# Kernel optimization log

Measured on AMD Instinct MI355X. Metric: run time of the kernel, lower is better.

## Reference

```python
import jax, jax.numpy as jnp
import numpy as np

NUM_GROUPS = 8
EPS = 1e-5


def setup_inputs() -> dict:
    key = jax.random.key(0)
    ks = jax.random.split(key, 3)
    B, C, H, W = 32, 256, 64, 64
    x = jax.random.normal(ks[0], (B, C, H, W), dtype=jnp.float32)
    gn_weight = jnp.ones((C,), dtype=jnp.float32)
    gn_bias = jnp.zeros((C,), dtype=jnp.float32)
    # 1x1 convs stored as [out_ch, in_ch] matrices (kernel dims squeezed)
    qkv_weight = jax.random.normal(ks[1], (3 * C, C), dtype=jnp.float32) * (1.0 / np.sqrt(C))
    qkv_bias = jnp.zeros((3 * C,), dtype=jnp.float32)
    proj_weight = jax.random.normal(ks[2], (C, C), dtype=jnp.float32) * (1.0 / np.sqrt(C))
    proj_bias = jnp.zeros((C,), dtype=jnp.float32)
    return {
        "x": x,
        "gn_weight": gn_weight,
        "gn_bias": gn_bias,
        "qkv_weight": qkv_weight,
        "qkv_bias": qkv_bias,
        "proj_weight": proj_weight,
        "proj_bias": proj_bias,
    }


def _group_norm(x, weight, bias):
    B, C, H, W = x.shape
    g = x.reshape(B, NUM_GROUPS, C // NUM_GROUPS, H, W)
    mean = g.mean(axis=(2, 3, 4), keepdims=True)
    var = g.var(axis=(2, 3, 4), keepdims=True)
    g = (g - mean) * jax.lax.rsqrt(var + EPS)
    x = g.reshape(B, C, H, W)
    return x * weight[None, :, None, None] + bias[None, :, None, None]


def reference(x, gn_weight, gn_bias, qkv_weight, qkv_bias, proj_weight, proj_bias):
    B, C, H, W = x.shape
    x_norm = _group_norm(x, gn_weight, gn_bias)
    # 1x1 conv C -> 3C: contraction over channel dim
    qkv = jnp.einsum('bchw,oc->bohw', x_norm, qkv_weight) + qkv_bias[None, :, None, None]
    qkv = qkv.reshape(B, 3, C, H * W)  # [B,3,C,HW]
    q, k, v = qkv[:, 0], qkv[:, 1], qkv[:, 2]  # each [B,C,HW]
    # channel attention: attn is [B,C,C], softmax over last (key-channel) dim
    scale = 1.0 / jnp.sqrt(jnp.asarray(C, dtype=x.dtype))
    scores = jnp.einsum('bcn,bdn->bcd', q, k) * scale
    attn = jax.nn.softmax(scores, axis=-1)
    out = jnp.einsum('bcd,bdn->bcn', attn, v).reshape(B, C, H, W)
    proj = jnp.einsum('bchw,oc->bohw', out, proj_weight) + proj_bias[None, :, None, None]
    return x + proj
```

## Files before the change

kernel.cpp:

```cpp
#include <hip/hip_runtime.h>


#define B_ 32
#define C_ 256
#define N_ 4096
#define GSIZE (32 * N_)
#define EPSV 1e-5f
#define SCALE 0.0625f

#define OFF_SC    0
#define OFF_SH    8192
#define OFF_RS    16384
#define OFF_RSP   24576
#define OFF_SQP   90112
#define OFF_RALL  155648
#define OFF_CV    180224
#define OFF_CONST 188416
#define OFF_WVT   196608
#define OFF_GM    229376
#define OFF_AT    2326528
#define OFF_S16   4423680
#define OFF_GP    5472256

typedef _Float16 half_t;
typedef half_t f16x8 __attribute__((ext_vector_type(8)));
typedef float f32x16 __attribute__((ext_vector_type(16)));

__global__ __launch_bounds__(512, 1) void gram_v4_k(const float* __restrict__ x,
                                                    float* __restrict__ ws) {
  __shared__ __align__(16) char hb[2][32768];
  int b = blockIdx.x >> 3, ks = blockIdx.x & 7;
  int t = threadIdx.x;
  const float* xb = x + (size_t)b * (C_ * (size_t)N_) + ks * 512;
  int lane = t & 63, w = t >> 6;
  int wm = w >> 2, wn = w & 3, r31 = lane & 31, hi = lane >> 5;
  int lrow = t >> 4, lc4 = t & 15;
  const float* lbase = xb + (size_t)lrow * N_ + lc4 * 4;
  f32x16 acc[4][2] = {};
  float4 stg[2][8];
  float rs[8] = {0.f, 0.f, 0.f, 0.f, 0.f, 0.f, 0.f, 0.f};
  float rq[8] = {0.f, 0.f, 0.f, 0.f, 0.f, 0.f, 0.f, 0.f};

#define LOADV(sb, c)                                                      \
  _Pragma("unroll") for (int p = 0; p < 8; ++p)                           \
      stg[sb][p] = *(const float4*)(lbase + (size_t)p * 32 * N_ + (c) * 64);

#define WRITEV(sb, buf)                                                   \
  {                                                                       \
    char* bp = hb[buf];                                                   \
    _Pragma("unroll") for (int p = 0; p < 8; ++p) {                       \
      float4 v = stg[sb][p];                                              \
      rs[p] += v.x + v.y + v.z + v.w;                                     \
      rq[p] += v.x * v.x + v.y * v.y + v.z * v.z + v.w * v.w;             \
      union { half_t h[4]; uint2 u; } H;                                  \
      H.h[0] = (half_t)v.x; H.h[1] = (half_t)v.y;                         \
      H.h[2] = (half_t)v.z; H.h[3] = (half_t)v.w;                         \
      int row = lrow + p * 32;                                            \
      int slot = (lc4 >> 1) ^ (row & 7);                                  \
      *(uint2*)(bp + row * 128 + slot * 16 + (lc4 & 1) * 8) = H.u;        \
    }                                                                     \
  }

  LOADV(0, 0);
  LOADV(1, 1);
  WRITEV(0, 0);
  __syncthreads();
  for (int c = 0; c < 8; ++c) {
    int buf = c & 1;
#pragma unroll
    for (int kk = 0; kk < 4; ++kk) {
      int kb = kk * 32 + hi * 16;
      f16x8 Af[4], Bf[2];
#pragma unroll
      for (int m = 0; m < 4; ++m) {
        int row = wm * 128 + m * 32 + r31;
        Af[m] = *(const f16x8*)(hb[buf] + row * 128 + (((kb >> 4) ^ (row & 7)) * 16));
      }
#pragma unroll
      for (int n = 0; n < 2; ++n) {
        int row = wn * 64 + n * 32 + r31;
        Bf[n] = *(const f16x8*)(hb[buf] + row * 128 + (((kb >> 4) ^ (row & 7)) * 16));
      }
#pragma unroll
      for (int m = 0; m < 4; ++m)
#pragma unroll
        for (int n = 0; n < 2; ++n)
          acc[m][n] = __builtin_amdgcn_mfma_f32_32x32x16_f16(Af[m], Bf[n], acc[m][n], 0, 0, 0);
    }
    if (c < 7) {
      int nb = (c + 1) & 1;
      WRITEV(nb, nb);
      if (c < 6) LOADV(buf, c + 2);
      __syncthreads();
    }
  }
#pragma unroll
  for (int p = 0; p < 8; ++p) {
    float s = rs[p], q = rq[p];
    s += __shfl_xor(s, 1); s += __shfl_xor(s, 2);
    s += __shfl_xor(s, 4); s += __shfl_xor(s, 8);
    q += __shfl_xor(q, 1); q += __shfl_xor(q, 2);
    q += __shfl_xor(q, 4); q += __shfl_xor(q, 8);
    if ((t & 15) == 0) {
      int row = lrow + p * 32;
      ws[OFF_RSP + (size_t)blockIdx.x * 256 + row] = s;
      ws[OFF_SQP + (size_t)blockIdx.x * 256 + row] = q;
    }
  }
  half_t* Gp = (half_t*)(ws + OFF_GP) + (size_t)blockIdx.x * 65536;
#pragma unroll
  for (int m = 0; m < 4; ++m)
#pragma unroll
    for (int n = 0; n < 2; ++n)
#pragma unroll
      for (int r = 0; r < 16; ++r) {
        int gr = wm * 128 + m * 32 + (r & 3) + 8 * (r >> 2) + 4 * hi;
        int gc = wn * 64 + n * 32 + r31;
        Gp[gr * 256 + gc] = (half_t)acc[m][n][r];
      }
#undef LOADV
#undef WRITEV
}

__global__ __launch_bounds__(256) void gsum_k(float* __restrict__ ws) {
  int bx = blockIdx.x;
  int b = bx >> 6, seg = bx & 63;
  int e0 = seg * 1024 + threadIdx.x * 4;
  const half_t* Gp = (const half_t*)(ws + OFF_GP) + (size_t)b * 8 * 65536 + e0;
  float4 s = {0.f, 0.f, 0.f, 0.f};
#pragma unroll
  for (int ks = 0; ks < 8; ++ks) {
    union { uint2 u; half_t h[4]; } P;
    P.u = *(const uint2*)(Gp + (size_t)ks * 65536);
    s.x += (float)P.h[0]; s.y += (float)P.h[1];
    s.z += (float)P.h[2]; s.w += (float)P.h[3];
  }
  *(float4*)(ws + OFF_GM + (size_t)b * 65536 + e0) = s;
}

__global__ __launch_bounds__(256) void prep_k(const float* __restrict__ gw,
                                              const float* __restrict__ gb,
                                              const float* __restrict__ qkvw,
                                              float* __restrict__ ws) {
  int b = blockIdx.x, t = threadIdx.x;
  __shared__ float sL[256], qL[256], svecs[256], gmean[8], grstd[8];
  float s = 0.f, q = 0.f;
#pragma unroll
  for (int ks = 0; ks < 8; ++ks) {
    s += ws[OFF_RSP + (b * 8 + ks) * 256 + t];
    q += ws[OFF_SQP + (b * 8 + ks) * 256 + t];
  }
  ws[OFF_RS + b * 256 + t] = s;
  sL[t] = s; qL[t] = q;
  __syncthreads();
  if (t < 8) {
    float gs = 0.f, gq = 0.f;
    for (int i = 0; i < 32; ++i) { gs += sL[t * 32 + i]; gq += qL[t * 32 + i]; }
    float mean = gs * (1.f / GSIZE);
    float var = gq * (1.f / GSIZE) - mean * mean;
    gmean[t] = mean;
    grstd[t] = rsqrtf(var + EPSV);
  }
  __syncthreads();
  int g = t >> 5;
  float sc = grstd[g] * gw[t];
  float sh = gb[t] - gmean[g] * sc;
  ws[OFF_SC + b * 256 + t] = sc;
  ws[OFF_SH + b * 256 + t] = sh;
  float sv = s * sc + 4096.f * sh;
  svecs[t] = sv;
  __syncthreads();
  for (int oo = 0; oo < 3; ++oo) {
    int o = t + oo * 256;
    const float* wr = qkvw + (size_t)o * 256;
    float acc = 0.f;
#pragma unroll 8
    for (int c = 0; c < 256; ++c) acc += wr[c] * svecs[c];
    ws[OFF_RALL + b * 768 + o] = acc;
  }
}

__global__ __launch_bounds__(256) void wvt_k(const float* __restrict__ qkvw,
                                             float* __restrict__ ws) {
  int e = blockIdx.x, d = threadIdx.x;
  float v = qkvw[(size_t)(512 + d) * 256 + e];
  ((half_t*)(ws + OFF_WVT))[e * 256 + d] = (half_t)v;
}

__global__ __launch_bounds__(256) void fused_logits_k(
    const float* __restrict__ qkvw, const float* __restrict__ qkvb,
    float* __restrict__ ws) {
  int b = blockIdx.y, r0 = blockIdx.x * 32;
  int t = threadIdx.x, lane = t & 63, w = t >> 6, r31 = lane & 31, hi = lane >> 5;
  __shared__ __align__(16) char GHL[32768];
  __shared__ __align__(16) char AHL[8192];
  __shared__ float T1s[32][257];
  __shared__ float scs[256], shs[256], rss[256];
  __shared__ float bk_s[256], rk_s[256], bq_s[32], rq_s[32];
  scs[t] = ws[OFF_SC + b * 256 + t];
  shs[t] = ws[OFF_SH + b * 256 + t];
  rss[t] = ws[OFF_RS + b * 256 + t];
  bk_s[t] = qkvb[256 + t];
  rk_s[t] = ws[OFF_RALL + b * 768 + 256 + t];
  if (t < 32) {
    bq_s[t] = qkvb[r0 + t];
    rq_s[t] = ws[OFF_RALL + b * 768 + r0 + t];
  }
  __syncthreads();
  const float* Graw = ws + OFF_GM + (size_t)b * 65536;
  f32x16 acc[2] = {};
  for (int k0 = 0; k0 < 256; k0 += 32) {
    {
      int row = t >> 3, c4 = t & 7;
      float4 v = *(const float4*)(qkvw + (size_t)(r0 + row) * 256 + k0 + c4 * 4);
      union { half_t h[4]; uint2 u; } H, L;
      float vv[4] = {v.x, v.y, v.z, v.w};
#pragma unroll
      for (int j = 0; j < 4; ++j) {
        half_t h = (half_t)vv[j];
        H.h[j] = h; L.h[j] = (half_t)(vv[j] - (float)h);
      }
      int s8 = row & 7;
      *(uint2*)(AHL + row * 128 + (((c4 >> 1) ^ s8) * 16) + (c4 & 1) * 8) = H.u;
      *(uint2*)(AHL + row * 128 + ((((c4 >> 1) + 4) ^ s8) * 16) + (c4 & 1) * 8) = L.u;
    }
    {
#pragma unroll
      for (int p = 0; p < 8; ++p) {
        int f = t + p * 256;
        int row = f >> 3, c4 = f & 7;
        float4 gv = *(const float4*)(Graw + (size_t)row * 256 + k0 + c4 * 4);
        float scd = scs[row], shd = shs[row], rsd = rss[row];
        union { half_t h[4]; uint2 u; } H, L;
        float gvv[4] = {gv.x, gv.y, gv.z, gv.w};
#pragma unroll
        for (int j = 0; j < 4; ++j) {
          int cc = k0 + c4 * 4 + j;
          float scc = scs[cc], shc = shs[cc];
          float val = scc * scd * gvv[j] + scc * shd * rss[cc] +
                      shc * scd * rsd + 4096.f * shc * shd;
          half_t h = (half_t)val;
          H.h[j] = h; L.h[j] = (half_t)(val - (float)h);
        }
        int s8 = row & 7;
        *(uint2*)(GHL + row * 128 + (((c4 >> 1) ^ s8) * 16) + (c4 & 1) * 8) = H.u;
        *(uint2*)(GHL + row * 128 + ((((c4 >> 1) + 4) ^ s8) * 16) + (c4 & 1) * 8) = L.u;
      }
    }
    __syncthreads();
#pragma unroll
    for (int kk = 0; kk < 2; ++kk) {
      int kb = kk * 32 + hi * 16;
      int arow = r31;
      f16x8 Aq = *(const f16x8*)(AHL + arow * 128 + (((kb >> 4) ^ (arow & 7)) * 16));
#pragma unroll
      for (int n = 0; n < 2; ++n) {
        int row = w * 64 + n * 32 + r31;
        int s8 = row & 7;
        f16x8 Bh = *(const f16x8*)(GHL + row * 128 + (((kb >> 4) ^ s8) * 16));
        f16x8 Bl = *(const f16x8*)(GHL + row * 128 + ((((kb >> 4) + 4) ^ s8) * 16));
        acc[n] = __builtin_amdgcn_mfma_f32_32x32x16_f16(Aq, Bh, acc[n], 0, 0, 0);
        acc[n] = __builtin_amdgcn_mfma_f32_32x32x16_f16(Aq, Bl, acc[n], 0, 0, 0);
      }
    }
    __syncthreads();
  }
#pragma unroll
  for (int n = 0; n < 2; ++n)
#pragma unroll
    for (int r = 0; r < 16; ++r)
      T1s[(r & 3) + 8 * (r >> 2) + 4 * hi][w * 64 + n * 32 + r31] = acc[n][r];
  __syncthreads();
  f32x16 acc2[2] = {};
  for (int k0 = 0; k0 < 256; k0 += 64) {
    {
      int row = t >> 3;
#pragma unroll
      for (int u = 0; u < 2; ++u) {
        int c4 = (t & 7) + u * 8;
        float vv[4];
#pragma unroll
        for (int j = 0; j < 4; ++j) vv[j] = T1s[row][k0 + c4 * 4 + j];
        union { half_t h[4]; uint2 u2; } H, L;
#pragma unroll
        for (int j = 0; j < 4; ++j) {
          half_t h = (half_t)vv[j];
          H.h[j] = h; L.h[j] = (half_t)(vv[j] - (float)h);
        }
        int s16 = row & 15;
        *(uint2*)(AHL + row * 256 + (((c4 >> 1) ^ s16) * 16) + (c4 & 1) * 8) = H.u2;
        *(uint2*)(AHL + row * 256 + ((((c4 >> 1) + 8) ^ s16) * 16) + (c4 & 1) * 8) = L.u2;
      }
    }
    {
#pragma unroll
      for (int p = 0; p < 16; ++p) {
        int f = t + p * 256;
        int row = f >> 4, c4 = f & 15;
        float4 v = *(const float4*)(qkvw + (size_t)(256 + row) * 256 + k0 + c4 * 4);
        union { half_t h[4]; uint2 u; } H;
        H.h[0] = (half_t)v.x; H.h[1] = (half_t)v.y;
        H.h[2] = (half_t)v.z; H.h[3] = (half_t)v.w;
        int slot = (c4 >> 1) ^ (row & 7);
        *(uint2*)(GHL + row * 128 + slot * 16 + (c4 & 1) * 8) = H.u;
      }
    }
    __syncthreads();
#pragma unroll
    for (int kk = 0; kk < 4; ++kk) {
      int kb = kk * 32 + hi * 16;
      int arow = r31;
      int s16 = arow & 15;
      f16x8 Ah = *(const f16x8*)(AHL + arow * 256 + (((kb >> 4) ^ s16) * 16));
      f16x8 Al = *(const f16x8*)(AHL + arow * 256 + ((((kb >> 4) + 8) ^ s16) * 16));
#pragma unroll
      for (int n = 0; n < 2; ++n) {
        int row = w * 64 + n * 32 + r31;
        f16x8 Bf = *(const f16x8*)(GHL + row * 128 + (((kb >> 4) ^ (row & 7)) * 16));
        acc2[n] = __builtin_amdgcn_mfma_f32_32x32x16_f16(Ah, Bf, acc2[n], 0, 0, 0);
        acc2[n] = __builtin_amdgcn_mfma_f32_32x32x16_f16(Al, Bf, acc2[n], 0, 0, 0);
      }
    }
    __syncthreads();
  }
#pragma unroll
  for (int n = 0; n < 2; ++n)
#pragma unroll
    for (int r = 0; r < 16; ++r) {
      int rr = (r & 3) + 8 * (r >> 2) + 4 * hi;
      int cc = w * 64 + n * 32 + r31;
      float v = acc2[n][r];
      v = (v + bq_s[rr] * rk_s[cc] + bk_s[cc] * rq_s[rr] +
           4096.f * bq_s[rr] * bk_s[cc]) * SCALE;
      T1s[rr][cc] = v;
    }
  __syncthreads();
  bk_s[t] = qkvb[512 + t];
  __syncthreads();
  {
    int row = t >> 3, ls = t & 7;
    float m = -1e30f;
#pragma unroll
    for (int i = 0; i < 32; ++i) m = fmaxf(m, T1s[row][ls + i * 8]);
    m = fmaxf(m, __shfl_xor(m, 1));
    m = fmaxf(m, __shfl_xor(m, 2));
    m = fmaxf(m, __shfl_xor(m, 4));
    float s = 0.f, cvp = 0.f;
#pragma unroll
    for (int i = 0; i < 32; ++i) {
      int col = ls + i * 8;
      float e = __expf(T1s[row][col] - m);
      T1s[row][col] = e;
      s += e;
      cvp += e * bk_s[col];
    }
    s += __shfl_xor(s, 1); s += __shfl_xor(s, 2); s += __shfl_xor(s, 4);
    cvp += __shfl_xor(cvp, 1); cvp += __shfl_xor(cvp, 2); cvp += __shfl_xor(cvp, 4);
    float inv = 1.f / s;
#pragma unroll
    for (int i = 0; i < 32; ++i) T1s[row][ls + i * 8] *= inv;
    if (ls == 0) ws[OFF_CV + b * 256 + r0 + row] = cvp * inv;
  }
  __syncthreads();
  {
    float* ATb = ws + OFF_AT + (size_t)b * 65536;
#pragma unroll
    for (int u = 0; u < 8; ++u) {
      float4 v = {T1s[u * 4 + 0][t], T1s[u * 4 + 1][t], T1s[u * 4 + 2][t],
                  T1s[u * 4 + 3][t]};
      *(float4*)(ATb + (size_t)t * 256 + r0 + u * 4) = v;
    }
  }
}

__global__ __launch_bounds__(256) void fused_s_k(const float* __restrict__ pw,
                                                 const float* __restrict__ pb,
                                                 float* __restrict__ ws) {
  int b = blockIdx.y, r0 = blockIdx.x * 32;
  int t = threadIdx.x, lane = t & 63, w = t >> 6, r31 = lane & 31, hi = lane >> 5;
  __shared__ __align__(16) char GHL[32768];
  __shared__ __align__(16) char AHL[8192];
  __shared__ float T1s[32][257];
  __shared__ float cvs[256], scv[256], shv[256];
  cvs[t] = ws[OFF_CV + b * 256 + t];
  scv[t] = ws[OFF_SC + b * 256 + t];
  shv[t] = ws[OFF_SH + b * 256 + t];
  __syncthreads();
  const float* ATb = ws + OFF_AT + (size_t)b * 65536;
  f32x16 acc[2] = {};
  for (int k0 = 0; k0 < 256; k0 += 64) {
    {
#pragma unroll
      for (int p = 0; p < 2; ++p) {
        int f = t + p * 256;
        int row = f >> 4, c4 = f & 15;
        float4 v = *(const float4*)(pw + (size_t)(r0 + row) * 256 + k0 + c4 * 4);
        union { half_t h[4]; uint2 u; } H;
        H.h[0] = (half_t)v.x; H.h[1] = (half_t)v.y;
        H.h[2] = (half_t)v.z; H.h[3] = (half_t)v.w;
        int slot = (c4 >> 1) ^ (row & 7);
        *(uint2*)(AHL + row * 128 + slot * 16 + (c4 & 1) * 8) = H.u;
      }
    }
    {
#pragma unroll
      for (int p = 0; p < 16; ++p) {
        int f = t + p * 256;
        int row = f >> 4, c4 = f & 15;
        float4 v = *(const float4*)(ATb + (size_t)row * 256 + k0 + c4 * 4);
        union { half_t h[4]; uint2 u; } H;
        H.h[0] = (half_t)v.x; H.h[1] = (half_t)v.y;
        H.h[2] = (half_t)v.z; H.h[3] = (half_t)v.w;
        int slot = (c4 >> 1) ^ (row & 7);
        *(uint2*)(GHL + row * 128 + slot * 16 + (c4 & 1) * 8) = H.u;
      }
    }
    __syncthreads();
#pragma unroll
    for (int kk = 0; kk < 4; ++kk) {
      int kb = kk * 32 + hi * 16;
      int arow = r31;
      f16x8 Af = *(const f16x8*)(AHL + arow * 128 + (((kb >> 4) ^ (arow & 7)) * 16));
#pragma unroll
      for (int n = 0; n < 2; ++n) {
        int row = w * 64 + n * 32 + r31;
        f16x8 Bf = *(const f16x8*)(GHL + row * 128 + (((kb >> 4) ^ (row & 7)) * 16));
        acc[n] = __builtin_amdgcn_mfma_f32_32x32x16_f16(Af, Bf, acc[n], 0, 0, 0);
      }
    }
    __syncthreads();
  }
#pragma unroll
  for (int n = 0; n < 2; ++n)
#pragma unroll
    for (int r = 0; r < 16; ++r)
      T1s[(r & 3) + 8 * (r >> 2) + 4 * hi][w * 64 + n * 32 + r31] = acc[n][r];
  __syncthreads();
  float cfull = 0.f;
  {
    int row = t >> 3, ls = t & 7;
    float a = 0.f;
#pragma unroll
    for (int i = 0; i < 32; ++i) {
      int c = ls + i * 8;
      a += pw[(size_t)(r0 + row) * 256 + c] * cvs[c];
    }
    a += __shfl_xor(a, 1); a += __shfl_xor(a, 2); a += __shfl_xor(a, 4);
    cfull = a + pb[r0 + row];
  }
  const half_t* WVT = (const half_t*)(ws + OFF_WVT);
  f32x16 acc2[2] = {};
  for (int k0 = 0; k0 < 256; k0 += 64) {
    {
      int row = t >> 3;
#pragma unroll
      for (int u = 0; u < 2; ++u) {
        int c4 = (t & 7) + u * 8;
        float vv[4];
#pragma unroll
        for (int j = 0; j < 4; ++j) vv[j] = T1s[row][k0 + c4 * 4 + j];
        union { half_t h[4]; uint2 u2; } H, L;
#pragma unroll
        for (int j = 0; j < 4; ++j) {
          half_t h = (half_t)vv[j];
          H.h[j] = h; L.h[j] = (half_t)(vv[j] - (float)h);
        }
        int s16 = row & 15;
        *(uint2*)(AHL + row * 256 + (((c4 >> 1) ^ s16) * 16) + (c4 & 1) * 8) = H.u2;
        *(uint2*)(AHL + row * 256 + ((((c4 >> 1) + 8) ^ s16) * 16) + (c4 & 1) * 8) = L.u2;
      }
    }
    {
#pragma unroll
      for (int p = 0; p < 8; ++p) {
        int f = t + p * 256;
        int row = f >> 3, h8 = f & 7;
        uint2 v = *(const uint2*)(WVT + (size_t)row * 256 + k0 + h8 * 8);
        uint2 v2 = *(const uint2*)(WVT + (size_t)row * 256 + k0 + h8 * 8 + 4);
        int slot = h8 ^ (row & 7);
        *(uint2*)(GHL + row * 128 + slot * 16) = v;
        *(uint2*)(GHL + row * 128 + slot * 16 + 8) = v2;
      }
    }
    __syncthreads();
#pragma unroll
    for (int kk = 0; kk < 4; ++kk) {
      int kb = kk * 32 + hi * 16;
      int arow = r31;
      int s16 = arow & 15;
      f16x8 Ah = *(const f16x8*)(AHL + arow * 256 + (((kb >> 4) ^ s16) * 16));
      f16x8 Al = *(const f16x8*)(AHL + arow * 256 + ((((kb >> 4) + 8) ^ s16) * 16));
#pragma unroll
      for (int n = 0; n < 2; ++n) {
        int row = w * 64 + n * 32 + r31;
        f16x8 Bf = *(const f16x8*)(GHL + row * 128 + (((kb >> 4) ^ (row & 7)) * 16));
        acc2[n] = __builtin_amdgcn_mfma_f32_32x32x16_f16(Ah, Bf, acc2[n], 0, 0, 0);
        acc2[n] = __builtin_amdgcn_mfma_f32_32x32x16_f16(Al, Bf, acc2[n], 0, 0, 0);
      }
    }
    __syncthreads();
  }
#pragma unroll
  for (int n = 0; n < 2; ++n)
#pragma unroll
    for (int r = 0; r < 16; ++r)
      T1s[(r & 3) + 8 * (r >> 2) + 4 * hi][w * 64 + n * 32 + r31] = acc2[n][r];
  __syncthreads();
  {
    half_t* Sb = (half_t*)(ws + OFF_S16) + (size_t)b * 65536;
    int row = t >> 3, seg = t & 7;
    float dsh = 0.f;
#pragma unroll
    for (int u = 0; u < 4; ++u) {
      union { half_t h[8]; uint4 v; } P;
#pragma unroll
      for (int j = 0; j < 8; ++j) {
        int col = seg * 32 + u * 8 + j;
        float sv = T1s[row][col];
        dsh += sv * shv[col];
        P.h[j] = (half_t)(sv * scv[col]);
      }
      *(uint4*)(Sb + (size_t)(r0 + row) * 256 + seg * 32 + u * 8) = P.v;
    }
    dsh += __shfl_xor(dsh, 1); dsh += __shfl_xor(dsh, 2); dsh += __shfl_xor(dsh, 4);
    if (seg == 0) ws[OFF_CONST + b * 256 + r0 + row] = cfull + dsh;
  }
}

__global__ __launch_bounds__(256, 3) void final_v2_k(
    const float* __restrict__ x, float* __restrict__ out,
    const float* __restrict__ ws) {
  __shared__ __align__(16) half_t xs[256 * 68];
  int b = blockIdx.y, n0 = blockIdx.x * 64;
  int t = threadIdx.x, lane = t & 63, w = t >> 6;
  int r31 = lane & 31, hi = lane >> 5;
  const half_t* Sb = (const half_t*)(ws + OFF_S16) + (size_t)b * 65536;
  const float* xb = x + (size_t)b * (C_ * (size_t)N_);
#pragma unroll
  for (int h = 0; h < 2; ++h) {
    float4 v[8];
#pragma unroll
    for (int p = 0; p < 8; ++p) {
      int f = t + (h * 8 + p) * 256;
      int c = f >> 4, q = f & 15;
      v[p] = *(const float4*)(xb + (size_t)c * N_ + n0 + q * 4);
    }
#pragma unroll
    for (int p = 0; p < 8; ++p) {
      int f = t + (h * 8 + p) * 256;
      int c = f >> 4, q = f & 15;
      union { half_t hh[4]; uint2 u; } H;
      H.hh[0] = (half_t)v[p].x; H.hh[1] = (half_t)v[p].y;
      H.hh[2] = (half_t)v[p].z; H.hh[3] = (half_t)v[p].w;
      *(uint2*)(&xs[c * 68 + q * 4]) = H.u;
    }
  }
  __syncthreads();
  f32x16 acc[2][2] = {};
  int obase = w * 64;
  f16x8 An[2];
#pragma unroll
  for (int m = 0; m < 2; ++m)
    An[m] = *(const f16x8*)(Sb + (size_t)(obase + m * 32 + r31) * 256 + hi * 8);
#pragma unroll 4
  for (int kk = 0; kk < 16; ++kk) {
    f16x8 Af[2] = {An[0], An[1]};
    if (kk < 15) {
      int cknx = (kk + 1) * 16 + hi * 8;
#pragma unroll
      for (int m = 0; m < 2; ++m)
        An[m] = *(const f16x8*)(Sb + (size_t)(obase + m * 32 + r31) * 256 + cknx);
    }
    int ck = kk * 16 + hi * 8;
    f16x8 Bf[2];
#pragma unroll
    for (int n = 0; n < 2; ++n) {
      int col = n * 32 + r31;
#pragma unroll
      for (int j = 0; j < 8; ++j) Bf[n][j] = xs[(ck + j) * 68 + col];
    }
#pragma unroll
    for (int m = 0; m < 2; ++m)
#pragma unroll
      for (int n = 0; n < 2; ++n)
        acc[m][n] = __builtin_amdgcn_mfma_f32_32x32x16_f16(Af[m], Bf[n], acc[m][n], 0, 0, 0);
  }
  float* ob = out + (size_t)b * (C_ * (size_t)N_);
  const float* cstb = ws + OFF_CONST + b * 256;
#pragma unroll
  for (int m = 0; m < 2; ++m)
#pragma unroll
    for (int r = 0; r < 16; ++r) {
      int o = obase + m * 32 + (r & 3) + 8 * (r >> 2) + 4 * hi;
      float cv = cstb[o];
      size_t base = (size_t)o * N_ + n0;
#pragma unroll
      for (int n = 0; n < 2; ++n) {
        int col = n * 32 + r31;
        ob[base + col] = acc[m][n][r] + xb[base + col] + cv;
      }
    }
}

extern "C" void kernel_launch(void* const* d_in, const int* in_sizes, int n_in,
                              void* d_out, int out_size, void* d_ws,
                              size_t ws_size, hipStream_t stream) {
  const float* x = (const float*)d_in[0];
  const float* gw = (const float*)d_in[1];
  const float* gb = (const float*)d_in[2];
  const float* qkvw = (const float*)d_in[3];
  const float* qkvb = (const float*)d_in[4];
  const float* pw = (const float*)d_in[5];
  const float* pb = (const float*)d_in[6];
  float* out = (float*)d_out;
  float* ws = (float*)d_ws;

  hipLaunchKernelGGL(gram_v4_k, dim3(256), dim3(512), 0, stream, x, ws);
  hipLaunchKernelGGL(prep_k, dim3(32), dim3(256), 0, stream, gw, gb, qkvw, ws);
  hipLaunchKernelGGL(gsum_k, dim3(2048), dim3(256), 0, stream, ws);
  hipLaunchKernelGGL(wvt_k, dim3(256), dim3(256), 0, stream, qkvw, ws);
  hipLaunchKernelGGL(fused_logits_k, dim3(8, 32), dim3(256), 0, stream, qkvw, qkvb, ws);
  hipLaunchKernelGGL(fused_s_k, dim3(8, 32), dim3(256), 0, stream, pw, pb, ws);
  hipLaunchKernelGGL(final_v2_k, dim3(64, 32), dim3(256), 0, stream, x, out, ws);
}
```

Baseline: 255.1 us.

## Fold group-norm affine into weights, pre-split Gram to f16, swizzle final LDS

The GroupNorm scale/shift is moved out of the per-element Gram correction. Q/K weights are pre-scaled by the per-channel scale, and the shift terms go into new rank-1 vectors (u, v) that prep computes and that are added in the logits epilogue. The Gram sum is stored directly as f16 hi/lo pairs, so logits loads it with plain vector copies instead of recomputing and splitting it. The V-weight transpose is tiled through shared memory, and the final GEMM uses a swizzled, transposed LDS layout with 16-byte vector reads and a deeper A prefetch. Dropping the low half of the weight split and changing launch bounds may reduce accuracy or change occupancy.

```diff
diff --git a/kernel.cpp b/kernel.cpp
--- a/kernel.cpp
+++ b/kernel.cpp
@@ -14,13 +14,15 @@
 #define OFF_RSP   24576
 #define OFF_SQP   90112
 #define OFF_RALL  155648
-#define OFF_CV    180224
-#define OFF_CONST 188416
-#define OFF_WVT   196608
-#define OFF_GM    229376
-#define OFF_AT    2326528
-#define OFF_S16   4423680
-#define OFF_GP    5472256
+#define OFF_UV    180224
+#define OFF_CV    212992
+#define OFF_CONST 221184
+#define OFF_WVT   229376
+#define OFF_GH    262144
+#define OFF_GL    1310720
+#define OFF_AT    2359296
+#define OFF_S16   4456448
+#define OFF_GP    5505024
 
 typedef _Float16 half_t;
 typedef half_t f16x8 __attribute__((ext_vector_type(8)));
@@ -122,28 +124,36 @@
 #undef WRITEV
 }
 
-__global__ __launch_bounds__(256) void gsum_k(float* __restrict__ ws) {
+__global__ __launch_bounds__(256) void gsum2_k(float* __restrict__ ws) {
   int bx = blockIdx.x;
   int b = bx >> 6, seg = bx & 63;
   int e0 = seg * 1024 + threadIdx.x * 4;
   const half_t* Gp = (const half_t*)(ws + OFF_GP) + (size_t)b * 8 * 65536 + e0;
-  float4 s = {0.f, 0.f, 0.f, 0.f};
+  float s[4] = {0.f, 0.f, 0.f, 0.f};
 #pragma unroll
   for (int ks = 0; ks < 8; ++ks) {
     union { uint2 u; half_t h[4]; } P;
     P.u = *(const uint2*)(Gp + (size_t)ks * 65536);
-    s.x += (float)P.h[0]; s.y += (float)P.h[1];
-    s.z += (float)P.h[2]; s.w += (float)P.h[3];
-  }
-  *(float4*)(ws + OFF_GM + (size_t)b * 65536 + e0) = s;
-}
-
-__global__ __launch_bounds__(256) void prep_k(const float* __restrict__ gw,
-                                              const float* __restrict__ gb,
-                                              const float* __restrict__ qkvw,
-                                              float* __restrict__ ws) {
+#pragma unroll
+    for (int i = 0; i < 4; ++i) s[i] += (float)P.h[i];
+  }
+  union { half_t h[4]; uint2 u; } H, L;
+#pragma unroll
+  for (int i = 0; i < 4; ++i) {
+    H.h[i] = (half_t)s[i];
+    L.h[i] = (half_t)(s[i] - (float)H.h[i]);
+  }
+  *(uint2*)((half_t*)(ws + OFF_GH) + (size_t)b * 65536 + e0) = H.u;
+  *(uint2*)((half_t*)(ws + OFF_GL) + (size_t)b * 65536 + e0) = L.u;
+}
+
+__global__ __launch_bounds__(256) void prep2_k(const float* __restrict__ gw,
+                                               const float* __restrict__ gb,
+                                               const float* __restrict__ qkvw,
+                                               float* __restrict__ ws) {
   int b = blockIdx.x, t = threadIdx.x;
-  __shared__ float sL[256], qL[256], svecs[256], gmean[8], grstd[8];
+  __shared__ float sL[256], qL[256], svecs[256], scrs[256], shsm[256];
+  __shared__ float gmean[8], grstd[8];
   float s = 0.f, q = 0.f;
 #pragma unroll
   for (int ks = 0; ks < 8; ++ks) {
@@ -167,27 +177,63 @@
   float sh = gb[t] - gmean[g] * sc;
   ws[OFF_SC + b * 256 + t] = sc;
   ws[OFF_SH + b * 256 + t] = sh;
-  float sv = s * sc + 4096.f * sh;
-  svecs[t] = sv;
-  __syncthreads();
-  for (int oo = 0; oo < 3; ++oo) {
-    int o = t + oo * 256;
-    const float* wr = qkvw + (size_t)o * 256;
-    float acc = 0.f;
-#pragma unroll 8
-    for (int c = 0; c < 256; ++c) acc += wr[c] * svecs[c];
-    ws[OFF_RALL + b * 768 + o] = acc;
-  }
-}
-
-__global__ __launch_bounds__(256) void wvt_k(const float* __restrict__ qkvw,
-                                             float* __restrict__ ws) {
-  int e = blockIdx.x, d = threadIdx.x;
-  float v = qkvw[(size_t)(512 + d) * 256 + e];
-  ((half_t*)(ws + OFF_WVT))[e * 256 + d] = (half_t)v;
-}
-
-__global__ __launch_bounds__(256) void fused_logits_k(
+  svecs[t] = s * sc + 4096.f * sh;
+  scrs[t] = s * sc;
+  shsm[t] = sh;
+  __syncthreads();
+  {
+    const float* r1 = qkvw + (size_t)t * 256;
+    float rq = 0.f, uq = 0.f, vq = 0.f;
+#pragma unroll 4
+    for (int c = 0; c < 256; ++c) {
+      float wv = r1[c];
+      rq += wv * svecs[c]; uq += wv * scrs[c]; vq += wv * shsm[c];
+    }
+    ws[OFF_RALL + b * 768 + t] = rq;
+    ws[OFF_UV + b * 1024 + t] = uq;
+    ws[OFF_UV + b * 1024 + 256 + t] = vq;
+  }
+  {
+    const float* r2 = qkvw + (size_t)(256 + t) * 256;
+    float rk = 0.f, uk = 0.f, vk = 0.f;
+#pragma unroll 4
+    for (int c = 0; c < 256; ++c) {
+      float wv = r2[c];
+      rk += wv * svecs[c]; uk += wv * scrs[c]; vk += wv * shsm[c];
+    }
+    ws[OFF_RALL + b * 768 + 256 + t] = rk;
+    ws[OFF_UV + b * 1024 + 512 + t] = uk;
+    ws[OFF_UV + b * 1024 + 768 + t] = vk;
+  }
+}
+
+__global__ __launch_bounds__(256) void wvt2_k(const float* __restrict__ qkvw,
+                                              float* __restrict__ ws) {
+  __shared__ float sm[64][68];
+  int be = blockIdx.x * 64, bd = blockIdx.y * 64;
+  int t = threadIdx.x;
+#pragma unroll
+  for (int i = 0; i < 4; ++i) {
+    int f = t + i * 256;
+    int row = f >> 4, c4 = f & 15;
+    float4 v = *(const float4*)(qkvw + (size_t)(512 + bd + row) * 256 + be + c4 * 4);
+    sm[row][c4 * 4 + 0] = v.x; sm[row][c4 * 4 + 1] = v.y;
+    sm[row][c4 * 4 + 2] = v.z; sm[row][c4 * 4 + 3] = v.w;
+  }
+  __syncthreads();
+  half_t* WVT = (half_t*)(ws + OFF_WVT);
+#pragma unroll
+  for (int i = 0; i < 4; ++i) {
+    int f = t + i * 256;
+    int el = f >> 4, d4 = (f & 15) * 4;
+    union { half_t h[4]; uint2 u; } P;
+#pragma unroll
+    for (int k = 0; k < 4; ++k) P.h[k] = (half_t)sm[d4 + k][el];
+    *(uint2*)(WVT + (size_t)(be + el) * 256 + bd + d4) = P.u;
+  }
+}
+
+__global__ __launch_bounds__(256) void logits2_k(
     const float* __restrict__ qkvw, const float* __restrict__ qkvb,
     float* __restrict__ ws) {
   int b = blockIdx.y, r0 = blockIdx.x * 32;
@@ -195,56 +241,44 @@
   __shared__ __align__(16) char GHL[32768];
   __shared__ __align__(16) char AHL[8192];
   __shared__ float T1s[32][257];
-  __shared__ float scs[256], shs[256], rss[256];
-  __shared__ float bk_s[256], rk_s[256], bq_s[32], rq_s[32];
+  __shared__ float scs[256];
+  __shared__ float bk_s[256], rk_s[256], uk_s[256], vk_s[256];
+  __shared__ float bq_s[32], rq_s[32], uq_s[32], vq_s[32];
   scs[t] = ws[OFF_SC + b * 256 + t];
-  shs[t] = ws[OFF_SH + b * 256 + t];
-  rss[t] = ws[OFF_RS + b * 256 + t];
   bk_s[t] = qkvb[256 + t];
   rk_s[t] = ws[OFF_RALL + b * 768 + 256 + t];
+  uk_s[t] = ws[OFF_UV + b * 1024 + 512 + t];
+  vk_s[t] = ws[OFF_UV + b * 1024 + 768 + t];
   if (t < 32) {
     bq_s[t] = qkvb[r0 + t];
     rq_s[t] = ws[OFF_RALL + b * 768 + r0 + t];
-  }
-  __syncthreads();
-  const float* Graw = ws + OFF_GM + (size_t)b * 65536;
+    uq_s[t] = ws[OFF_UV + b * 1024 + r0 + t];
+    vq_s[t] = ws[OFF_UV + b * 1024 + 256 + r0 + t];
+  }
+  __syncthreads();
+  const half_t* Gh = (const half_t*)(ws + OFF_GH) + (size_t)b * 65536;
+  const half_t* Gl = (const half_t*)(ws + OFF_GL) + (size_t)b * 65536;
   f32x16 acc[2] = {};
   for (int k0 = 0; k0 < 256; k0 += 32) {
     {
       int row = t >> 3, c4 = t & 7;
       float4 v = *(const float4*)(qkvw + (size_t)(r0 + row) * 256 + k0 + c4 * 4);
-      union { half_t h[4]; uint2 u; } H, L;
-      float vv[4] = {v.x, v.y, v.z, v.w};
-#pragma unroll
-      for (int j = 0; j < 4; ++j) {
-        half_t h = (half_t)vv[j];
-        H.h[j] = h; L.h[j] = (half_t)(vv[j] - (float)h);
-      }
+      union { half_t h[4]; uint2 u; } H;
+      H.h[0] = (half_t)(v.x * scs[k0 + c4 * 4 + 0]);
+      H.h[1] = (half_t)(v.y * scs[k0 + c4 * 4 + 1]);
+      H.h[2] = (half_t)(v.z * scs[k0 + c4 * 4 + 2]);
+      H.h[3] = (half_t)(v.w * scs[k0 + c4 * 4 + 3]);
       int s8 = row & 7;
       *(uint2*)(AHL + row * 128 + (((c4 >> 1) ^ s8) * 16) + (c4 & 1) * 8) = H.u;
-      *(uint2*)(AHL + row * 128 + ((((c4 >> 1) + 4) ^ s8) * 16) + (c4 & 1) * 8) = L.u;
     }
     {
 #pragma unroll
       for (int p = 0; p < 8; ++p) {
         int f = t + p * 256;
-        int row = f >> 3, c4 = f & 7;
-        float4 gv = *(const float4*)(Graw + (size_t)row * 256 + k0 + c4 * 4);
-        float scd = scs[row], shd = shs[row], rsd = rss[row];
-        union { half_t h[4]; uint2 u; } H, L;
-        float gvv[4] = {gv.x, gv.y, gv.z, gv.w};
-#pragma unroll
-        for (int j = 0; j < 4; ++j) {
-          int cc = k0 + c4 * 4 + j;
-          float scc = scs[cc], shc = shs[cc];
-          float val = scc * scd * gvv[j] + scc * shd * rss[cc] +
-                      shc * scd * rsd + 4096.f * shc * shd;
-          half_t h = (half_t)val;
-          H.h[j] = h; L.h[j] = (half_t)(val - (float)h);
-        }
-        int s8 = row & 7;
-        *(uint2*)(GHL + row * 128 + (((c4 >> 1) ^ s8) * 16) + (c4 & 1) * 8) = H.u;
-        *(uint2*)(GHL + row * 128 + ((((c4 >> 1) + 4) ^ s8) * 16) + (c4 & 1) * 8) = L.u;
+        int row = f >> 3, ko = f & 7;
+        const half_t* src = (ko < 4) ? Gh : Gl;
+        uint4 v = *(const uint4*)(src + (size_t)row * 256 + k0 + (ko & 3) * 8);
+        *(uint4*)(GHL + row * 128 + ((ko ^ (row & 7)) * 16)) = v;
       }
     }
     __syncthreads();
@@ -299,8 +333,10 @@
         int row = f >> 4, c4 = f & 15;
         float4 v = *(const float4*)(qkvw + (size_t)(256 + row) * 256 + k0 + c4 * 4);
         union { half_t h[4]; uint2 u; } H;
-        H.h[0] = (half_t)v.x; H.h[1] = (half_t)v.y;
-        H.h[2] = (half_t)v.z; H.h[3] = (half_t)v.w;
+        H.h[0] = (half_t)(v.x * scs[k0 + c4 * 4 + 0]);
+        H.h[1] = (half_t)(v.y * scs[k0 + c4 * 4 + 1]);
+        H.h[2] = (half_t)(v.z * scs[k0 + c4 * 4 + 2]);
+        H.h[3] = (half_t)(v.w * scs[k0 + c4 * 4 + 3]);
         int slot = (c4 >> 1) ^ (row & 7);
         *(uint2*)(GHL + row * 128 + slot * 16 + (c4 & 1) * 8) = H.u;
       }
@@ -330,8 +366,9 @@
       int rr = (r & 3) + 8 * (r >> 2) + 4 * hi;
       int cc = w * 64 + n * 32 + r31;
       float v = acc2[n][r];
-      v = (v + bq_s[rr] * rk_s[cc] + bk_s[cc] * rq_s[rr] +
-           4096.f * bq_s[rr] * bk_s[cc]) * SCALE;
+      float ukv = uk_s[cc] + 4096.f * vk_s[cc];
+      v = (v + uq_s[rr] * vk_s[cc] + vq_s[rr] * ukv + bq_s[rr] * rk_s[cc] +
+           bk_s[cc] * (rq_s[rr] + 4096.f * bq_s[rr])) * SCALE;
       T1s[rr][cc] = v;
     }
   __syncthreads();
@@ -527,57 +564,64 @@
   }
 }
 
-__global__ __launch_bounds__(256, 3) void final_v2_k(
+__global__ __launch_bounds__(256) void final_v3_k(
     const float* __restrict__ x, float* __restrict__ out,
     const float* __restrict__ ws) {
-  __shared__ __align__(16) half_t xs[256 * 68];
+  __shared__ __align__(16) char xs[32768];
   int b = blockIdx.y, n0 = blockIdx.x * 64;
   int t = threadIdx.x, lane = t & 63, w = t >> 6;
   int r31 = lane & 31, hi = lane >> 5;
   const half_t* Sb = (const half_t*)(ws + OFF_S16) + (size_t)b * 65536;
   const float* xb = x + (size_t)b * (C_ * (size_t)N_);
-#pragma unroll
-  for (int h = 0; h < 2; ++h) {
-    float4 v[8];
-#pragma unroll
-    for (int p = 0; p < 8; ++p) {
-      int f = t + (h * 8 + p) * 256;
-      int c = f >> 4, q = f & 15;
-      v[p] = *(const float4*)(xb + (size_t)c * N_ + n0 + q * 4);
-    }
-#pragma unroll
-    for (int p = 0; p < 8; ++p) {
-      int f = t + (h * 8 + p) * 256;
-      int c = f >> 4, q = f & 15;
-      union { half_t hh[4]; uint2 u; } H;
-      H.hh[0] = (half_t)v[p].x; H.hh[1] = (half_t)v[p].y;
-      H.hh[2] = (half_t)v[p].z; H.hh[3] = (half_t)v[p].w;
-      *(uint2*)(&xs[c * 68 + q * 4]) = H.u;
+  {
+    int n4 = (t & 15) * 4, cb = (t >> 4) * 4;
+#pragma unroll
+    for (int p = 0; p < 4; ++p) {
+      int c = cb + p * 64;
+      float a[4][4];
+#pragma unroll
+      for (int i = 0; i < 4; ++i) {
+        float4 v = *(const float4*)(xb + (size_t)(c + i) * N_ + n0 + n4);
+        a[i][0] = v.x; a[i][1] = v.y; a[i][2] = v.z; a[i][3] = v.w;
+      }
+      int gbase = (c >> 3) << 4, off8 = (c & 7) * 2;
+#pragma unroll
+      for (int j = 0; j < 4; ++j) {
+        int n = n4 + j;
+        union { half_t h[4]; uint2 u; } P;
+        P.h[0] = (half_t)a[0][j]; P.h[1] = (half_t)a[1][j];
+        P.h[2] = (half_t)a[2][j]; P.h[3] = (half_t)a[3][j];
+        *(uint2*)(xs + n * 512 + (gbase ^ ((n & 7) << 4)) + off8) = P.u;
+      }
     }
   }
   __syncthreads();
   f32x16 acc[2][2] = {};
   int obase = w * 64;
-  f16x8 An[2];
-#pragma unroll
-  for (int m = 0; m < 2; ++m)
-    An[m] = *(const f16x8*)(Sb + (size_t)(obase + m * 32 + r31) * 256 + hi * 8);
-#pragma unroll 4
+  const half_t* Arow0 = Sb + (size_t)(obase + r31) * 256;
+  const half_t* Arow1 = Sb + (size_t)(obase + 32 + r31) * 256;
+  f16x8 An0[2], An1[2];
+  An0[0] = *(const f16x8*)(Arow0 + hi * 8);
+  An0[1] = *(const f16x8*)(Arow1 + hi * 8);
+  An1[0] = *(const f16x8*)(Arow0 + 16 + hi * 8);
+  An1[1] = *(const f16x8*)(Arow1 + 16 + hi * 8);
+#pragma unroll
   for (int kk = 0; kk < 16; ++kk) {
-    f16x8 Af[2] = {An[0], An[1]};
-    if (kk < 15) {
-      int cknx = (kk + 1) * 16 + hi * 8;
-#pragma unroll
-      for (int m = 0; m < 2; ++m)
-        An[m] = *(const f16x8*)(Sb + (size_t)(obase + m * 32 + r31) * 256 + cknx);
+    f16x8 Af[2];
+    if (kk & 1) { Af[0] = An1[0]; Af[1] = An1[1]; }
+    else        { Af[0] = An0[0]; Af[1] = An0[1]; }
+    if (kk < 14) {
+      int ck2 = (kk + 2) * 16 + hi * 8;
+      if (kk & 1) { An1[0] = *(const f16x8*)(Arow0 + ck2); An1[1] = *(const f16x8*)(Arow1 + ck2); }
+      else        { An0[0] = *(const f16x8*)(Arow0 + ck2); An0[1] = *(const f16x8*)(Arow1 + ck2); }
     }
     int ck = kk * 16 + hi * 8;
+    int gsel = (ck >> 3) << 4;
     f16x8 Bf[2];
 #pragma unroll
     for (int n = 0; n < 2; ++n) {
       int col = n * 32 + r31;
-#pragma unroll
-      for (int j = 0; j < 8; ++j) Bf[n][j] = xs[(ck + j) * 68 + col];
+      Bf[n] = *(const f16x8*)(xs + col * 512 + (gsel ^ ((col & 7) << 4)));
     }
 #pragma unroll
     for (int m = 0; m < 2; ++m)
@@ -616,10 +660,10 @@
   float* ws = (float*)d_ws;
 
   hipLaunchKernelGGL(gram_v4_k, dim3(256), dim3(512), 0, stream, x, ws);
-  hipLaunchKernelGGL(prep_k, dim3(32), dim3(256), 0, stream, gw, gb, qkvw, ws);
-  hipLaunchKernelGGL(gsum_k, dim3(2048), dim3(256), 0, stream, ws);
-  hipLaunchKernelGGL(wvt_k, dim3(256), dim3(256), 0, stream, qkvw, ws);
-  hipLaunchKernelGGL(fused_logits_k, dim3(8, 32), dim3(256), 0, stream, qkvw, qkvb, ws);
+  hipLaunchKernelGGL(prep2_k, dim3(32), dim3(256), 0, stream, gw, gb, qkvw, ws);
+  hipLaunchKernelGGL(gsum2_k, dim3(2048), dim3(256), 0, stream, ws);
+  hipLaunchKernelGGL(wvt2_k, dim3(4, 4), dim3(256), 0, stream, qkvw, ws);
+  hipLaunchKernelGGL(logits2_k, dim3(8, 32), dim3(256), 0, stream, qkvw, qkvb, ws);
   hipLaunchKernelGGL(fused_s_k, dim3(8, 32), dim3(256), 0, stream, pw, pb, ws);
-  hipLaunchKernelGGL(final_v2_k, dim3(64, 32), dim3(256), 0, stream, x, out, ws);
-}
+  hipLaunchKernelGGL(final_v3_k, dim3(64, 32), dim3(256), 0, stream, x, out, ws);
+}
```

Result: faster. 240.4 us (-5.8%).
